# Kernel tuning notes

Measured on AMD Instinct MI355X. Metric: run time of the kernel, lower is better.

The kernel has to match this reference:

```python
import jax, jax.numpy as jnp
import numpy as np
import math

B, N = 16, 32            # batch, num_agents
D_OBS = 128              # obs_input_dim
N_ACT = 16               # num_actions
D_OA_IN = D_OBS + N_ACT  # obs_act_input_dim = 144
D_OUT = 128              # obs_output_dim == obs_act_output_dim
HID = 64                 # final hidden
FINAL_OUT = 1


def _xavier(k, shape):
    fan_out, fan_in = shape
    lim = math.sqrt(6.0 / (fan_in + fan_out))
    return jax.random.uniform(k, shape, jnp.float32, -lim, lim)


def setup_inputs() -> dict:
    key = jax.random.key(0)
    ks = jax.random.split(key, 12)
    return {
        "states": jax.random.normal(ks[0], (B, N, D_OBS), jnp.float32),
        "policies": jax.random.uniform(ks[1], (B, N, N_ACT), jnp.float32),
        "actions": jax.random.uniform(ks[2], (B, N, N_ACT), jnp.float32),
        # uniform noise in [0,1); forward applies (noise-0.5)*0.1 like torch.rand path
        "noise": jax.random.uniform(ks[3], (B, N, N, N, D_OUT), jnp.float32),
        # torch Linear weights: [out_features, in_features], bias=False
        "Wk_oa": _xavier(ks[4], (D_OUT, D_OA_IN)),
        "Wq_oa": _xavier(ks[5], (D_OUT, D_OA_IN)),
        "Wv_oa": _xavier(ks[6], (D_OUT, D_OA_IN)),
        "Wk_o": _xavier(ks[7], (D_OUT, D_OBS)),
        "Wq_o": _xavier(ks[8], (D_OUT, D_OBS)),
        "Wv_o": _xavier(ks[9], (D_OUT, D_OBS)),
        "W1": _xavier(ks[10], (HID, 2 * D_OUT)),
        "W2": _xavier(ks[11], (FINAL_OUT, HID)),
    }


def reference(states, policies, actions, noise, Wk_oa, Wq_oa, Wv_oa, Wk_o, Wq_o, Wv_o, W1, W2):
    n = states.shape[1]
    d_oa = Wk_oa.shape[0]
    d_o = Wk_o.shape[0]

    obs_actions = jnp.concatenate([states, actions], axis=-1)   # [B,N,D_oa_in]
    obs_policy = jnp.concatenate([states, policies], axis=-1)

    # --- obs-action attention branch ---
    K = obs_actions @ Wk_oa.T                                   # [B,N,d]
    Q = obs_actions @ Wq_oa.T
    # bmm(Q,K^T).transpose(1,2): score_t[b,j,i] = Q_i . K_j; softmax over i
    score_t = jnp.einsum('bid,bjd->bji', Q, K)
    w_oa = jax.nn.softmax(score_t / jnp.sqrt(jnp.asarray(d_oa, states.dtype)), axis=-1)  # [B,N,N]

    # place_policies/place_actions: diagonal picks obs_policy, off-diag obs_actions
    eye = jnp.eye(n, dtype=states.dtype)[None, :, :, None]       # [1,N,N,1]
    oap = eye * obs_policy[:, None, :, :] + (1.0 - eye) * obs_actions[:, None, :, :]  # [B,N,N,D_oa_in]
    AV = oap @ Wv_oa.T                                           # [B,N,N,d]

    # mean_i( AV[b,j,i,:] * w_oa[b,k,i] + (noise-0.5)*0.1 ); mean is linear -> split
    noise_mean = jnp.mean((noise - 0.5) * 0.1, axis=-2)          # [B,N,N,d]
    wav = jnp.einsum('bjid,bki->bkjd', AV, w_oa) / n + noise_mean  # [B,N,N,d]

    # --- obs-only attention branch ---
    Ko = states @ Wk_o.T
    Qo = states @ Wq_o.T
    AVO = states @ Wv_o.T                                        # [B,N,d]
    score_o = jnp.einsum('bid,bjd->bji', Qo, Ko)
    w_o = jax.nn.softmax(score_o / jnp.sqrt(jnp.asarray(d_o, states.dtype)), axis=-1)  # [B,N,N]
    wfo = jnp.einsum('bji,bid->bjd', w_o, AVO) / n               # [B,N,d]
    wfo_b = jnp.broadcast_to(wfo[:, :, None, :], wav.shape[:3] + (d_o,))  # [B,N,N,d]

    node = jnp.concatenate([wfo_b, wav], axis=-1)                # [B,N,N,2d]
    h = jax.nn.leaky_relu(node @ W1.T, negative_slope=0.01)
    value = h @ W2.T                                             # [B,N,N,1]
    return (value, w_oa, w_o[..., None])
```

## Files before the change

kernel.cpp:

```cpp
#include <hip/hip_runtime.h>


#define WS_K    0
#define WS_Q    65536
#define WS_VA   131072
#define WS_KO   196608
#define WS_QO   262144
#define WS_AVO  327680
#define WS_SDIV 393216
#define WS_DDIV 458752
#define WS_U    524288
#define WS_WOA  557056

__global__ __launch_bounds__(256) void k_transforms(
    const float* __restrict__ states, const float* __restrict__ policies,
    const float* __restrict__ actions,
    const float* __restrict__ Wk_oa, const float* __restrict__ Wq_oa,
    const float* __restrict__ Wv_oa, const float* __restrict__ Wk_o,
    const float* __restrict__ Wq_o,  const float* __restrict__ Wv_o,
    float* __restrict__ ws)
{
    __shared__ __align__(16) float xa[144];
    const int row = blockIdx.x;
    const int t = threadIdx.x;
    if (t < 128)       xa[t] = states[row * 128 + t];
    else if (t < 144)  xa[t] = actions[row * 16 + (t - 128)];
    __syncthreads();

    for (int u = t; u < 768; u += 256) {
        const int m = u >> 7, o = u & 127;
        const float* Wrow; int len4; float* dst;
        switch (m) {
            case 0: Wrow = Wk_oa + o * 144; len4 = 36; dst = ws + WS_K;  break;
            case 1: Wrow = Wq_oa + o * 144; len4 = 36; dst = ws + WS_Q;  break;
            case 2: Wrow = Wv_oa + o * 144; len4 = 36; dst = ws + WS_VA; break;
            case 3: Wrow = Wk_o  + o * 128; len4 = 32; dst = ws + WS_KO; break;
            case 4: Wrow = Wq_o  + o * 128; len4 = 32; dst = ws + WS_QO; break;
            default:Wrow = Wv_o  + o * 128; len4 = 32; dst = ws + WS_AVO;break;
        }
        const float4* W4 = (const float4*)Wrow;
        const float4* x4 = (const float4*)xa;
        float acc = 0.f;
        for (int c = 0; c < len4; ++c) {
            float4 w = W4[c], x = x4[c];
            acc += w.x * x.x + w.y * x.y + w.z * x.z + w.w * x.w;
        }
        dst[row * 128 + o] = acc;
    }
}

__global__ __launch_bounds__(256) void k_attn(
    const float* __restrict__ policies, const float* __restrict__ actions,
    const float* __restrict__ Wv_oa, const float* __restrict__ W1,
    float* __restrict__ ws, float* __restrict__ out)
{
    const float* K   = ws + WS_K;
    const float* Q   = ws + WS_Q;
    const float* Va  = ws + WS_VA;
    const float* Ko  = ws + WS_KO;
    const float* Qo  = ws + WS_QO;
    const float* AVO = ws + WS_AVO;
    float* Sdiv = ws + WS_SDIV;
    float* Ddiv = ws + WS_DDIV;
    float* U    = ws + WS_U;
    float* Woa  = ws + WS_WOA;

    const int b = blockIdx.x >> 5, r = blockIdx.x & 31;
    const int t = threadIdx.x;
    const int br = b * 32 + r;

    __shared__ __align__(16) float kr[128], kor[128], wfo[128];
    __shared__ float sA[32], sO[32], woa[32], wo[32], pd[16];

    if (t < 128) { kr[t] = K[br * 128 + t]; kor[t] = Ko[br * 128 + t]; }
    else if (t < 144) {
        int c = t - 128;
        pd[c] = policies[br * 16 + c] - actions[br * 16 + c];
    }
    __syncthreads();

    {
        const int i = t >> 3, seg = t & 7;
        const float4* q4  = (const float4*)(Q  + (b * 32 + i) * 128) + seg * 4;
        const float4* qo4 = (const float4*)(Qo + (b * 32 + i) * 128) + seg * 4;
        const float4* k4  = (const float4*)kr  + seg * 4;
        const float4* ko4 = (const float4*)kor + seg * 4;
        float a0 = 0.f, a1 = 0.f;
        #pragma unroll
        for (int c = 0; c < 4; ++c) {
            float4 q = q4[c], kk = k4[c];
            a0 += q.x * kk.x + q.y * kk.y + q.z * kk.z + q.w * kk.w;
            float4 p = qo4[c], mm = ko4[c];
            a1 += p.x * mm.x + p.y * mm.y + p.z * mm.z + p.w * mm.w;
        }
        #pragma unroll
        for (int off = 1; off < 8; off <<= 1) {
            a0 += __shfl_xor(a0, off, 64);
            a1 += __shfl_xor(a1, off, 64);
        }
        if (seg == 0) {
            const float scale = 0.08838834764831845f;
            sA[i] = a0 * scale;
            sO[i] = a1 * scale;
        }
    }
    __syncthreads();

    if (t < 64) {
        const int i = t & 31;
        float s = (t < 32) ? sA[i] : sO[i];
        float m = s;
        #pragma unroll
        for (int off = 1; off < 32; off <<= 1) m = fmaxf(m, __shfl_xor(m, off, 64));
        float e = __expf(s - m);
        float sum = e;
        #pragma unroll
        for (int off = 1; off < 32; off <<= 1) sum += __shfl_xor(sum, off, 64);
        float w = e / sum;
        if (t < 32) { woa[i] = w; out[16384 + br * 32 + i] = w; Woa[br * 32 + i] = w; }
        else        { wo[i]  = w; out[32768 + br * 32 + i] = w; }
    }
    __syncthreads();

    {
        const int d = t & 127;
        const float* M  = (t < 128) ? Va  : AVO;
        const float* wp = (t < 128) ? woa : wo;
        float acc = 0.f;
        #pragma unroll 8
        for (int i = 0; i < 32; ++i) acc += wp[i] * M[(b * 32 + i) * 128 + d];
        if (t < 128) {
            Sdiv[br * 128 + d] = acc * (1.f / 32.f);
            const float4* wv4 = (const float4*)(Wv_oa + d * 144 + 128);
            float dv = 0.f;
            #pragma unroll
            for (int c = 0; c < 4; ++c) {
                float4 w = wv4[c];
                dv += w.x * pd[4*c] + w.y * pd[4*c+1] + w.z * pd[4*c+2] + w.w * pd[4*c+3];
            }
            Ddiv[br * 128 + d] = dv * (1.f / 32.f);
        } else {
            wfo[d] = acc * (1.f / 32.f);
        }
    }
    __syncthreads();

    {
        const int h = t >> 2, q = t & 3;
        const float4* w4 = (const float4*)(W1 + h * 256) + q * 8;
        const float4* f4 = (const float4*)wfo + q * 8;
        float acc = 0.f;
        #pragma unroll
        for (int c = 0; c < 8; ++c) {
            float4 w = w4[c], f = f4[c];
            acc += w.x * f.x + w.y * f.y + w.z * f.z + w.w * f.w;
        }
        acc += __shfl_xor(acc, 1, 64);
        acc += __shfl_xor(acc, 2, 64);
        if (q == 0) U[br * 64 + h] = acc;
    }
}

__global__ __launch_bounds__(256) void k_value(
    const float* __restrict__ noise, const float* __restrict__ ws,
    const float* __restrict__ W1, const float* __restrict__ W2,
    float* __restrict__ out)
{
    const float* Sdiv = ws + WS_SDIV;
    const float* Ddiv = ws + WS_DDIV;
    const float* U    = ws + WS_U;
    const float* Woa  = ws + WS_WOA;

    const int blk = blockIdx.x;
    const int b  = blk >> 6;
    const int k  = (blk >> 1) & 31;
    const int j0 = (blk & 1) * 16;
    const int t  = threadIdx.x;
    const int h  = t >> 2, q = t & 3;
    const int lane = t & 63, wv = t >> 6;
    const int bk = b * 32 + k;

    __shared__ __align__(16) float part[512];
    __shared__ __align__(16) float wav_s[4 * 36];
    __shared__ float sdiv_s[128];
    __shared__ float woa_s[16];
    __shared__ float wsum[4];

    float w1r[32];
    {
        const float4* p = (const float4*)(W1 + h * 256 + 128 + q * 32);
        #pragma unroll
        for (int c = 0; c < 8; ++c) {
            float4 v = p[c];
            w1r[4*c] = v.x; w1r[4*c+1] = v.y; w1r[4*c+2] = v.z; w1r[4*c+3] = v.w;
        }
    }
    const float u_h  = U[bk * 64 + h];
    const float w2_h = W2[h];
    if (t < 128) sdiv_s[t] = Sdiv[bk * 128 + t];
    if (t < 16)  woa_s[t]  = Woa[bk * 32 + j0 + t];
    __syncthreads();

    const float4* nbase = (const float4*)noise + (size_t)(bk * 32) * 1024;

    float4 n0, n1, n2, n3;
    {
        const float4* p = nbase + (size_t)j0 * 1024 + t;
        n0 = p[0]; n1 = p[256]; n2 = p[512]; n3 = p[768];
    }
    for (int jj = 0; jj < 16; ++jj) {
        const int j = j0 + jj;
        float4 m0{}, m1{}, m2{}, m3{};
        if (jj < 15) {
            const float4* p = nbase + (size_t)(j + 1) * 1024 + t;
            m0 = p[0]; m1 = p[256]; m2 = p[512]; m3 = p[768];
        }
        float s0 = n0.x + n1.x + n2.x + n3.x;
        float s1 = n0.y + n1.y + n2.y + n3.y;
        float s2 = n0.z + n1.z + n2.z + n3.z;
        float s3 = n0.w + n1.w + n2.w + n3.w;
        s0 += __shfl_xor(s0, 32, 64);
        s1 += __shfl_xor(s1, 32, 64);
        s2 += __shfl_xor(s2, 32, 64);
        s3 += __shfl_xor(s3, 32, 64);
        if (lane < 32) {
            float4 v; v.x = s0; v.y = s1; v.z = s2; v.w = s3;
            ((float4*)part)[wv * 32 + lane] = v;
        }
        __syncthreads();
        if (t < 128) {
            float ns = part[t] + part[128 + t] + part[256 + t] + part[384 + t];
            float dv = Ddiv[(b * 32 + j) * 128 + t];
            float w  = sdiv_s[t] + dv * woa_s[jj] + ns * (0.1f / 32.f) - 0.05f;
            wav_s[(t >> 5) * 36 + (t & 31)] = w;
        }
        __syncthreads();
        {
            const float4* wv4 = (const float4*)(wav_s + q * 36);
            float acc = 0.f;
            #pragma unroll
            for (int c = 0; c < 8; ++c) {
                float4 v = wv4[c];
                acc += w1r[4*c] * v.x + w1r[4*c+1] * v.y
                     + w1r[4*c+2] * v.z + w1r[4*c+3] * v.w;
            }
            acc += __shfl_xor(acc, 1, 64);
            acc += __shfl_xor(acc, 2, 64);
            float hv = u_h + acc;
            hv = (hv > 0.f) ? hv : 0.01f * hv;
            float vp = (q == 0) ? hv * w2_h : 0.f;
            #pragma unroll
            for (int off = 4; off < 64; off <<= 1) vp += __shfl_xor(vp, off, 64);
            if (lane == 0) wsum[wv] = vp;
        }
        __syncthreads();
        if (t == 0) out[bk * 32 + j] = wsum[0] + wsum[1] + wsum[2] + wsum[3];
        n0 = m0; n1 = m1; n2 = m2; n3 = m3;
    }
}

extern "C" void kernel_launch(void* const* d_in, const int* in_sizes, int n_in,
                              void* d_out, int out_size, void* d_ws, size_t ws_size,
                              hipStream_t stream) {
    const float* states   = (const float*)d_in[0];
    const float* policies = (const float*)d_in[1];
    const float* actions  = (const float*)d_in[2];
    const float* noise    = (const float*)d_in[3];
    const float* Wk_oa    = (const float*)d_in[4];
    const float* Wq_oa    = (const float*)d_in[5];
    const float* Wv_oa    = (const float*)d_in[6];
    const float* Wk_o     = (const float*)d_in[7];
    const float* Wq_o     = (const float*)d_in[8];
    const float* Wv_o     = (const float*)d_in[9];
    const float* W1       = (const float*)d_in[10];
    const float* W2       = (const float*)d_in[11];
    float* out = (float*)d_out;
    float* ws  = (float*)d_ws;

    k_transforms<<<512, 256, 0, stream>>>(states, policies, actions,
                                          Wk_oa, Wq_oa, Wv_oa, Wk_o, Wq_o, Wv_o, ws);
    k_attn<<<512, 256, 0, stream>>>(policies, actions, Wv_oa, W1, ws, out);
    k_value<<<1024, 256, 0, stream>>>(noise, ws, W1, W2, out);
}
```

Baseline: 417.2 us.

## Restructure noise reduction in k_value to cut block barriers per iteration

Remaps threads so each wave reduces noise over i with intra-wave shuffles, which removes the shared partial-sum buffer and one barrier. The per-j Ddiv rows are prefetched into shared memory, wav is double-buffered, and the final per-wave sums go to the output through atomicAdd instead of a third barrier. The output is zeroed in the earlier kernel to support the atomics. This cuts three block barriers per iteration to one, at the cost of extra shuffles, atomics and a larger LDS footprint.

Result: no change. 417.1 us, median of 2 (-0.0%).

```diff
diff --git a/kernel.cpp b/kernel.cpp
--- a/kernel.cpp
+++ b/kernel.cpp
@@ -72,6 +72,7 @@
     __shared__ __align__(16) float kr[128], kor[128], wfo[128];
     __shared__ float sA[32], sO[32], woa[32], wo[32], pd[16];
 
+    if (t < 32) out[br * 32 + t] = 0.f;
     if (t < 128) { kr[t] = K[br * 128 + t]; kor[t] = Ko[br * 128 + t]; }
     else if (t < 144) {
         int c = t - 128;
@@ -146,9 +147,9 @@
     __syncthreads();
 
     {
-        const int h = t >> 2, q = t & 3;
-        const float4* w4 = (const float4*)(W1 + h * 256) + q * 8;
-        const float4* f4 = (const float4*)wfo + q * 8;
+        const int h = t >> 2, qq = t & 3;
+        const float4* w4 = (const float4*)(W1 + h * 256) + qq * 8;
+        const float4* f4 = (const float4*)wfo + qq * 8;
         float acc = 0.f;
         #pragma unroll
         for (int c = 0; c < 8; ++c) {
@@ -157,7 +158,7 @@
         }
         acc += __shfl_xor(acc, 1, 64);
         acc += __shfl_xor(acc, 2, 64);
-        if (q == 0) U[br * 64 + h] = acc;
+        if (qq == 0) U[br * 64 + h] = acc;
     }
 }
 
@@ -176,15 +177,14 @@
     const int k  = (blk >> 1) & 31;
     const int j0 = (blk & 1) * 16;
     const int t  = threadIdx.x;
+    const int l  = t & 63, wv = t >> 6;
     const int h  = t >> 2, q = t & 3;
-    const int lane = t & 63, wv = t >> 6;
     const int bk = b * 32 + k;
 
-    __shared__ __align__(16) float part[512];
-    __shared__ __align__(16) float wav_s[4 * 36];
-    __shared__ float sdiv_s[128];
+    __shared__ __align__(16) float wavs[2][4][36];
+    __shared__ __align__(16) float sdiv_s[128];
+    __shared__ __align__(16) float ddiv_s[16 * 128];
     __shared__ float woa_s[16];
-    __shared__ float wsum[4];
 
     float w1r[32];
     {
@@ -197,64 +197,78 @@
     }
     const float u_h  = U[bk * 64 + h];
     const float w2_h = W2[h];
-    if (t < 128) sdiv_s[t] = Sdiv[bk * 128 + t];
-    if (t < 16)  woa_s[t]  = Woa[bk * 32 + j0 + t];
-    __syncthreads();
-
-    const float4* nbase = (const float4*)noise + (size_t)(bk * 32) * 1024;
+
+    if (t < 32) ((float4*)sdiv_s)[t] = ((const float4*)(Sdiv + bk * 128))[t];
+    {
+        const float4* dsrc = (const float4*)(Ddiv + (b * 32 + j0) * 128);
+        ((float4*)ddiv_s)[t]       = dsrc[t];
+        ((float4*)ddiv_s)[t + 256] = dsrc[t + 256];
+    }
+    if (t < 16) woa_s[t] = Woa[bk * 32 + j0 + t];
+    __syncthreads();
+
+    const int d4 = (wv << 3) + (l & 7);
+    const int i0 = l >> 3;
+    const float4* nb = (const float4*)noise + (size_t)bk * 32768 + (size_t)(i0 * 32 + d4);
 
     float4 n0, n1, n2, n3;
     {
-        const float4* p = nbase + (size_t)j0 * 1024 + t;
+        const float4* p = nb + (size_t)j0 * 1024;
         n0 = p[0]; n1 = p[256]; n2 = p[512]; n3 = p[768];
     }
+    #pragma unroll 2
     for (int jj = 0; jj < 16; ++jj) {
         const int j = j0 + jj;
         float4 m0{}, m1{}, m2{}, m3{};
         if (jj < 15) {
-            const float4* p = nbase + (size_t)(j + 1) * 1024 + t;
+            const float4* p = nb + (size_t)(j + 1) * 1024;
             m0 = p[0]; m1 = p[256]; m2 = p[512]; m3 = p[768];
         }
-        float s0 = n0.x + n1.x + n2.x + n3.x;
-        float s1 = n0.y + n1.y + n2.y + n3.y;
-        float s2 = n0.z + n1.z + n2.z + n3.z;
-        float s3 = n0.w + n1.w + n2.w + n3.w;
-        s0 += __shfl_xor(s0, 32, 64);
-        s1 += __shfl_xor(s1, 32, 64);
-        s2 += __shfl_xor(s2, 32, 64);
-        s3 += __shfl_xor(s3, 32, 64);
-        if (lane < 32) {
-            float4 v; v.x = s0; v.y = s1; v.z = s2; v.w = s3;
-            ((float4*)part)[wv * 32 + lane] = v;
-        }
-        __syncthreads();
-        if (t < 128) {
-            float ns = part[t] + part[128 + t] + part[256 + t] + part[384 + t];
-            float dv = Ddiv[(b * 32 + j) * 128 + t];
-            float w  = sdiv_s[t] + dv * woa_s[jj] + ns * (0.1f / 32.f) - 0.05f;
-            wav_s[(t >> 5) * 36 + (t & 31)] = w;
-        }
-        __syncthreads();
+        float sx = n0.x + n1.x + n2.x + n3.x;
+        float sy = n0.y + n1.y + n2.y + n3.y;
+        float sz = n0.z + n1.z + n2.z + n3.z;
+        float sw = n0.w + n1.w + n2.w + n3.w;
+        #pragma unroll
+        for (int off = 8; off < 64; off <<= 1) {
+            sx += __shfl_xor(sx, off, 64);
+            sy += __shfl_xor(sy, off, 64);
+            sz += __shfl_xor(sz, off, 64);
+            sw += __shfl_xor(sw, off, 64);
+        }
+        const float woaj = woa_s[jj];
+        if (l < 8) {
+            const int db = (wv << 5) + (l << 2);
+            float4 w;
+            w.x = sdiv_s[db+0] + ddiv_s[jj*128+db+0] * woaj + sx * (0.1f/32.f) - 0.05f;
+            w.y = sdiv_s[db+1] + ddiv_s[jj*128+db+1] * woaj + sy * (0.1f/32.f) - 0.05f;
+            w.z = sdiv_s[db+2] + ddiv_s[jj*128+db+2] * woaj + sz * (0.1f/32.f) - 0.05f;
+            w.w = sdiv_s[db+3] + ddiv_s[jj*128+db+3] * woaj + sw * (0.1f/32.f) - 0.05f;
+            *(float4*)&wavs[jj & 1][wv][l << 2] = w;
+        }
+        asm volatile("s_waitcnt lgkmcnt(0)" ::: "memory");
+        __builtin_amdgcn_s_barrier();
+        __builtin_amdgcn_sched_barrier(0);
         {
-            const float4* wv4 = (const float4*)(wav_s + q * 36);
+            const float4* w4 = (const float4*)&wavs[jj & 1][q][0];
             float acc = 0.f;
             #pragma unroll
             for (int c = 0; c < 8; ++c) {
-                float4 v = wv4[c];
+                float4 v = w4[c];
                 acc += w1r[4*c] * v.x + w1r[4*c+1] * v.y
                      + w1r[4*c+2] * v.z + w1r[4*c+3] * v.w;
             }
             acc += __shfl_xor(acc, 1, 64);
             acc += __shfl_xor(acc, 2, 64);
-            float hv = u_h + acc;
-            hv = (hv > 0.f) ? hv : 0.01f * hv;
-            float vp = (q == 0) ? hv * w2_h : 0.f;
+            float vp = 0.f;
+            if (q == 0) {
+                float hv = u_h + acc;
+                hv = (hv > 0.f) ? hv : 0.01f * hv;
+                vp = hv * w2_h;
+            }
             #pragma unroll
             for (int off = 4; off < 64; off <<= 1) vp += __shfl_xor(vp, off, 64);
-            if (lane == 0) wsum[wv] = vp;
-        }
-        __syncthreads();
-        if (t == 0) out[bk * 32 + j] = wsum[0] + wsum[1] + wsum[2] + wsum[3];
+            if (l == 0) atomicAdd(out + bk * 32 + j, vp);
+        }
         n0 = m0; n1 = m1; n2 = m2; n3 = m3;
     }
 }
```
